# Kernel optimization log

Hardware: AMD Instinct MI355X
Metric: run time of the kernel (lower is better)

Reference implementation:

```python
import jax, jax.numpy as jnp
import numpy as np

# MANO fingertip / palm prior vertex indices from contact_loss
_F1 = [697,698,699,700,712,713,714,715,737,738,739,740,741,743,744,745,746,748,749,750,753,754,755,756,757,758,759,760,761,762,763,764,765,766,767,768]
_F2 = [46,47,48,49,164,165,166,167,194,195,223,237,238,280,281,298,301,317,320,323,324,325,326,327,328,329,330,331,332,333,340,341,342,343,344,345,346,347,348,349,350,351,352,353,354,355]
_F3 = [356,357,358,359,375,376,386,387,396,397,402,403,413,429,433,434,435,436,437,438,439,440,441,442,443,444,452,453,454,455,456,459,460,461,462,463,464,465,466,467]
_F4 = [468,469,470,471,484,485,486,496,497,506,507,513,514,524,545,546,547,548,549,550,551,552,553,555,563,564,565,566,567,570,572,573,574,575,576,577,578]
_F5 = [580,581,582,583,600,601,602,614,615,624,625,630,631,641,663,664,665,666,667,668,670,672,680,681,682,683,684,686,687,688,689,690,691,692,693,694,695]
_F0 = [73,96,98,99,772,774,775,777]
PRIOR_IDX = np.array(_F1 + _F2 + _F3 + _F4 + _F5 + _F0, dtype=np.int32)

KL_COEF = 0.005
A_W, B_W, C_W, D_W, E_W = 1.0, 0.1, 1000.0, 10.0, 10.0  # init kwargs a..e


def _nn(src, trg):
    """Brute-force 1-NN: src [B,N1,3] -> trg [B,N2,3].
    Returns (sq_dist [B,N1], idx [B,N1], diff src-near [B,N1,3])."""
    d2 = (jnp.sum(src * src, -1)[:, :, None]
          + jnp.sum(trg * trg, -1)[:, None, :]
          - 2.0 * jnp.einsum('bnd,bmd->bnm', src, trg))  # [B,N1,N2]
    idx = jnp.argmin(d2, axis=-1)
    near = jnp.take_along_axis(trg, idx[:, :, None], axis=1)
    diff = src - near
    return jnp.sum(diff * diff, axis=-1), idx, diff


def _p2p_signed(x, y, x_normals):
    """point2point_signed(x, y, x_normals): signed dist y->x, unsigned x->y."""
    _, yidx, y2x = _nn(y, x)  # nearest x for each y
    y_nn_normal = jnp.take_along_axis(x_normals, yidx[:, :, None], axis=1)
    in_out = jnp.sign(jnp.sum(y_nn_normal * y2x, axis=-1))
    y2x_signed = jnp.sqrt(jnp.sum(y2x * y2x, axis=-1)) * in_out  # [B,P2]
    _, _, x2y = _nn(x, y)  # nearest y for each x
    x2y_dist = jnp.sqrt(jnp.sum(x2y * x2y, axis=-1))  # [B,P1]
    return y2x_signed, x2y_dist


def _forward(recon_xyz, gt_xyz, recon_normals, gt_normals, obj_xyz, mean, log_var, v_weights):
    B = recon_xyz.shape[0]
    f32 = recon_xyz.dtype
    # --- CVAE recon (L2) + KLD ---
    recon_loss = jnp.sum((recon_xyz - gt_xyz) ** 2) / B
    kld = -0.5 * jnp.sum(1.0 + log_var - mean ** 2 - jnp.exp(log_var)) / B * 10.0
    # --- obj -> hand NN (squared dists, pytorch3d knn_points convention) ---
    recon_d2, recon_idx, _ = _nn(obj_xyz, recon_xyz)  # [B,3000]
    gt_d2, _, _ = _nn(obj_xyz, gt_xyz)
    # --- contact map from GT NN dist thresholding ---
    cmap = jnp.sqrt(gt_d2) < 0.005  # [B,3000] bool
    # --- contact_loss: obj NN to prior (fingertip/palm) recon verts ---
    prior = recon_xyz[:, PRIOR_IDX, :]
    obj_cd, _, _ = _nn(obj_xyz, prior)
    n_pts = jnp.sum(cmap.astype(f32))
    contact = 3000.0 * jnp.where(n_pts > 0, jnp.sum(obj_cd * cmap) / (B * n_pts), 0.0)
    # --- CMap_consistency_loss ---
    recon_cmap = jnp.sqrt(recon_d2) < 0.005
    consistency = -5.0 * jnp.sum((recon_cmap & cmap).astype(f32)) / (n_pts + 1e-4)
    # --- inter_penetr_loss: interior obj points via NN-normal dot sign ---
    nn_hand = jnp.take_along_axis(recon_xyz, recon_idx[:, :, None], axis=1)
    nn_normal = jnp.take_along_axis(recon_normals, recon_idx[:, :, None], axis=1)
    interior = jnp.sum((nn_hand - obj_xyz) * nn_normal, axis=-1) > 0
    penetr = 100.0 * jnp.sum(recon_d2 * interior) / B
    # --- loss_cnet: signed chamfer consistency ---
    vw2 = v_weights ** (1.0 / 2.5)
    o2h, h2o = _p2p_signed(recon_xyz, obj_xyz, recon_normals)
    o2h_gt, h2o_gt = _p2p_signed(gt_xyz, obj_xyz, gt_normals)
    w_dist = (o2h_gt < 0.01) & (o2h_gt > -0.005)
    w_neg = o2h < 0.0
    w = jnp.where(w_neg, 1.5, jnp.where(w_dist, 1.0, 0.1))
    loss_h = 35.0 * (1.0 - KL_COEF) * jnp.mean(jnp.abs(jnp.abs(h2o) - jnp.abs(h2o_gt)) * vw2)
    loss_o = 30.0 * (1.0 - KL_COEF) * jnp.mean(jnp.abs(o2h - o2h_gt) * w)
    cnet = loss_h + loss_o
    return (A_W * recon_loss + B_W * kld + C_W * penetr
            + D_W * contact + E_W * consistency + cnet)


def setup_inputs() -> dict:
    key = jax.random.key(0)
    ks = jax.random.split(key, 8)
    B, NH, NO, Z = 32, 778, 3000, 64
    s = 0.05  # meter-scale point clouds so contact thresholds (5mm) are meaningful
    def unit(k, shape):
        v = jax.random.normal(k, shape, dtype=jnp.float32)
        return v / jnp.linalg.norm(v, axis=-1, keepdims=True)
    return {
        'recon_xyz': jax.random.normal(ks[0], (B, NH, 3), dtype=jnp.float32) * s,
        'gt_xyz': jax.random.normal(ks[1], (B, NH, 3), dtype=jnp.float32) * s,
        'recon_normals': unit(ks[2], (B, NH, 3)),
        'gt_normals': unit(ks[3], (B, NH, 3)),
        'obj_xyz': jax.random.normal(ks[4], (B, NO, 3), dtype=jnp.float32) * s,
        'mean': jax.random.normal(ks[5], (B, Z), dtype=jnp.float32),
        'log_var': jax.random.normal(ks[6], (B, Z), dtype=jnp.float32) * 0.1,
        'v_weights': jax.random.uniform(ks[7], (NH,), dtype=jnp.float32),
    }


def reference(recon_xyz, gt_xyz, recon_normals, gt_normals, obj_xyz, mean, log_var, v_weights):
    return _forward(recon_xyz, gt_xyz, recon_normals, gt_normals, obj_xyz, mean, log_var, v_weights)
```

## Files before the change

### kernel.cpp

```cpp
#include <hip/hip_runtime.h>
#include <math.h>


#define NB 32
#define NH 778
#define NO 3000
#define NZ 64
#define NP 204

#define P_OBJ 4
#define OBJ_PTS 1024
#define OBJ_TILES 3

#define T2 12
#define FIN_OBJ_BLKS (NB * T2)
#define FIN_TAIL_BLKS ((NB * NH + 255) / 256)
#define FIN_BLKS (FIN_OBJ_BLKS + FIN_TAIL_BLKS)

#define NKEY (NB * NO)
#define NHT  (NB * NH)

#define ACC_STRIDE 32
#define ACC_SLOTS 16
#define ACC_FLOATS (ACC_SLOTS * ACC_STRIDE)

typedef unsigned int uint32;

__device__ __constant__ int c_prior[NP] = {
  697,698,699,700,712,713,714,715,737,738,739,740,741,743,744,745,746,748,749,750,
  753,754,755,756,757,758,759,760,761,762,763,764,765,766,767,768,
  46,47,48,49,164,165,166,167,194,195,223,237,238,280,281,298,301,317,320,323,
  324,325,326,327,328,329,330,331,332,333,340,341,342,343,344,345,346,347,348,349,
  350,351,352,353,354,355,
  356,357,358,359,375,376,386,387,396,397,402,403,413,429,433,434,435,436,437,438,
  439,440,441,442,443,444,452,453,454,455,456,459,460,461,462,463,464,465,466,467,
  468,469,470,471,484,485,486,496,497,506,507,513,514,524,545,546,547,548,549,550,
  551,552,553,555,563,564,565,566,567,570,572,573,574,575,576,577,578,
  580,581,582,583,600,601,602,614,615,624,625,630,631,641,663,664,665,666,667,668,
  670,672,680,681,682,683,684,686,687,688,689,690,691,692,693,694,695,
  73,96,98,99,772,774,775,777
};

__device__ __constant__ int c_prior_sorted[NP] = {
  46,47,48,49,73,96,98,99,164,165,166,167,194,
  195,223,237,238,280,281,298,301,317,320,323,324,325,326,327,328,329,330,331,
  332,333,340,341,342,343,344,345,346,347,348,349,350,351,352,353,354,355,356,
  357,358,359,375,376,386,387,
  396,397,402,403,413,429,433,434,435,436,437,438,439,440,441,442,443,444,452,
  453,454,455,456,459,460,461,462,463,464,465,466,467,468,469,470,471,484,485,
  486,496,497,506,507,513,514,524,545,546,547,548,549,550,551,552,553,555,563,
  564,565,566,567,570,572,573,574,575,576,577,578,580,581,582,583,
  600,601,602,614,615,624,625,630,631,641,663,664,665,666,667,668,670,672,680,
  681,682,683,684,686,687,688,689,690,691,692,693,694,695,697,698,699,700,712,
  713,714,715,737,738,739,740,741,743,744,745,746,748,749,750,753,754,755,756,
  757,758,759,760,761,762,763,764,765,766,767,768,772,774,775,777
};
__device__ __constant__ int c_psplit4[5] = {0, 13, 58, 131, 204};
__device__ __constant__ int c_psplit8[9] = {0, 6, 14, 19, 58, 97, 131, 154, 204};

__device__ inline float wave_sum(float v) {
  v += __shfl_down(v, 32);
  v += __shfl_down(v, 16);
  v += __shfl_down(v, 8);
  v += __shfl_down(v, 4);
  v += __shfl_down(v, 2);
  v += __shfl_down(v, 1);
  return v;
}

__device__ __forceinline__ float f_min3(float a, float b, float c) {
  float r;
  asm("v_min3_f32 %0, %1, %2, %3" : "=v"(r) : "v"(a), "v"(b), "v"(c));
  return r;
}
__device__ __forceinline__ float f_packao(float t, int j, uint32 mask) {
  float r;
  asm("v_and_or_b32 %0, %1, %2, %3" : "=v"(r) : "v"(t), "s"(mask), "v"(j));
  return r;
}

template<int JS, int JC, int HCn, int HCSn>
__global__ __launch_bounds__(256) void mega1t(
    const float* __restrict__ recon, const float* __restrict__ gt,
    const float* __restrict__ obj,
    float* __restrict__ keyR, float* __restrict__ keyG,
    float* __restrict__ priorK,
    float* __restrict__ minHR, float* __restrict__ minHG,
    float* __restrict__ accs)
{
  const int OBJ_B = NB * OBJ_TILES * JS;
  const int bid = blockIdx.x;
  const int tid = threadIdx.x;
  const uint32 KMASK = 0xFFFFFC00u;

  if (bid == 0) {
    accs[tid] = 0.0f;
    accs[tid + 256] = 0.0f;
  }

  if (bid < OBJ_B) {
    __shared__ float4 shA[JC];
    __shared__ float4 shB[JC];
    const int b     = bid / (OBJ_TILES * JS);
    const int rem   = bid % (OBJ_TILES * JS);
    const int tile  = rem / JS;
    const int split = rem % JS;
    const int jbase = split * JC;
    const int jcnt  = (NH - jbase < JC) ? (NH - jbase) : JC;

    for (int i = tid; i < jcnt; i += 256) {
      const float* p = recon + ((size_t)b * NH + jbase + i) * 3;
      float x = p[0], y = p[1], z = p[2];
      shA[i] = make_float4(x, y, z, x*x + y*y + z*z);
      const float* q = gt + ((size_t)b * NH + jbase + i) * 3;
      float gx = q[0], gy = q[1], gz = q[2];
      shB[i] = make_float4(gx, gy, gz, gx*gx + gy*gy + gz*gz);
    }
    __syncthreads();

    float nx[P_OBJ], ny[P_OBJ], nz[P_OBJ];
    int ob[P_OBJ]; bool val[P_OBJ];
    #pragma unroll
    for (int m = 0; m < P_OBJ; ++m) {
      int o = tile * OBJ_PTS + m * 256 + tid;
      ob[m] = o; val[m] = (o < NO);
      float x = 0.f, y = 0.f, z = 0.f;
      if (val[m]) {
        const float* op = obj + ((size_t)b * NO + o) * 3;
        x = op[0]; y = op[1]; z = op[2];
      }
      nx[m] = -2.f * x; ny[m] = -2.f * y; nz[m] = -2.f * z;
    }

    float bR[P_OBJ], bG[P_OBJ];
    #pragma unroll
    for (int m = 0; m < P_OBJ; ++m) { bR[m] = 3.4e38f; bG[m] = 3.4e38f; }

#define RSTEP(hh0, hh1, jj0, jj1) \
    { _Pragma("unroll") for (int m = 0; m < P_OBJ; ++m) { \
        float t0 = fmaf(nx[m], hh0.x, hh0.w); t0 = fmaf(ny[m], hh0.y, t0); t0 = fmaf(nz[m], hh0.z, t0); \
        float t1 = fmaf(nx[m], hh1.x, hh1.w); t1 = fmaf(ny[m], hh1.y, t1); t1 = fmaf(nz[m], hh1.z, t1); \
        bR[m] = f_min3(bR[m], f_packao(t0, jj0, KMASK), f_packao(t1, jj1, KMASK)); } }
#define GSTEP(gg0, gg1, jj0, jj1) \
    { _Pragma("unroll") for (int m = 0; m < P_OBJ; ++m) { \
        float u0 = fmaf(nx[m], gg0.x, gg0.w); u0 = fmaf(ny[m], gg0.y, u0); u0 = fmaf(nz[m], gg0.z, u0); \
        float u1 = fmaf(nx[m], gg1.x, gg1.w); u1 = fmaf(ny[m], gg1.y, u1); u1 = fmaf(nz[m], gg1.z, u1); \
        bG[m] = f_min3(bG[m], f_packao(u0, jj0, KMASK), f_packao(u1, jj1, KMASK)); } }

    float4 h0 = shA[0], h1 = shA[1];
    int i = 0;
    for (; i + 3 < jcnt; i += 2) {
      float4 g0 = shB[i], g1 = shB[i + 1];
      RSTEP(h0, h1, jbase + i, jbase + i + 1);
      float4 hn0 = shA[i + 2], hn1 = shA[i + 3];
      GSTEP(g0, g1, jbase + i, jbase + i + 1);
      h0 = hn0; h1 = hn1;
    }
    {
      float4 g0 = shB[i], g1 = shB[i + 1];
      RSTEP(h0, h1, jbase + i, jbase + i + 1);
      GSTEP(g0, g1, jbase + i, jbase + i + 1);
      i += 2;
    }
    for (; i < jcnt; ++i) {
      float4 hh = shA[i], gg = shB[i];
      #pragma unroll
      for (int m = 0; m < P_OBJ; ++m) {
        float t0 = fmaf(nx[m], hh.x, hh.w); t0 = fmaf(ny[m], hh.y, t0); t0 = fmaf(nz[m], hh.z, t0);
        bR[m] = fminf(bR[m], f_packao(t0, jbase + i, KMASK));
        float u0 = fmaf(nx[m], gg.x, gg.w); u0 = fmaf(ny[m], gg.y, u0); u0 = fmaf(nz[m], gg.z, u0);
        bG[m] = fminf(bG[m], f_packao(u0, jbase + i, KMASK));
      }
    }
#undef RSTEP
#undef GSTEP

    float bP[P_OBJ];
    #pragma unroll
    for (int m = 0; m < P_OBJ; ++m) bP[m] = 3.4e38f;
    const int* psp = (JS == 8) ? c_psplit8 : c_psplit4;
    const int pk0 = psp[split], pk1 = psp[split + 1];
    int k = pk0;
    for (; k + 1 < pk1; k += 2) {
      float4 ha = shA[c_prior_sorted[k] - jbase];
      float4 hb = shA[c_prior_sorted[k + 1] - jbase];
      #pragma unroll
      for (int m = 0; m < P_OBJ; ++m) {
        float t = fmaf(nx[m], ha.x, ha.w); t = fmaf(ny[m], ha.y, t); t = fmaf(nz[m], ha.z, t);
        float u = fmaf(nx[m], hb.x, hb.w); u = fmaf(ny[m], hb.y, u); u = fmaf(nz[m], hb.z, u);
        bP[m] = f_min3(bP[m], t, u);
      }
    }
    if (k < pk1) {
      float4 ha = shA[c_prior_sorted[k] - jbase];
      #pragma unroll
      for (int m = 0; m < P_OBJ; ++m) {
        float t = fmaf(nx[m], ha.x, ha.w); t = fmaf(ny[m], ha.y, t); t = fmaf(nz[m], ha.z, t);
        bP[m] = fminf(bP[m], t);
      }
    }

    #pragma unroll
    for (int m = 0; m < P_OBJ; ++m) {
      if (!val[m]) continue;
      const size_t idx = (size_t)split * NKEY + (size_t)b * NO + ob[m];
      keyR[idx] = bR[m];
      keyG[idx] = bG[m];
      priorK[idx] = bP[m];
    }
  } else {
    __shared__ float4 sO[HCSn];
    const int bid2 = bid - OBJ_B;
    const int oc = bid2 % HCn;
    const int b  = bid2 / HCn;

    const float* Ob = obj + ((size_t)b * NO + oc * HCSn) * 3;
    for (int i2 = tid; i2 < HCSn; i2 += 256) {
      float x = Ob[3*i2], y = Ob[3*i2+1], z = Ob[3*i2+2];
      sO[i2] = make_float4(x, y, z, x*x + y*y + z*z);
    }
    __syncthreads();

    float nrx[3], nry[3], nrz[3];
    float ngx[3], ngy[3], ngz[3];
    #pragma unroll
    for (int m = 0; m < 3; ++m) {
      const int j = m * 256 + tid;
      const float* rp = recon + ((size_t)b * NH + j) * 3;
      const float* gp = gt    + ((size_t)b * NH + j) * 3;
      nrx[m] = -2.f*rp[0]; nry[m] = -2.f*rp[1]; nrz[m] = -2.f*rp[2];
      ngx[m] = -2.f*gp[0]; ngy[m] = -2.f*gp[1]; ngz[m] = -2.f*gp[2];
    }

    float mR[3], mG[3];
    #pragma unroll
    for (int m = 0; m < 3; ++m) { mR[m] = 3.4e38f; mG[m] = 3.4e38f; }

#define HSTEP(oo0, oo1) \
    { _Pragma("unroll") for (int m = 0; m < 3; ++m) { \
        float t0 = fmaf(nrx[m], oo0.x, oo0.w); t0 = fmaf(nry[m], oo0.y, t0); t0 = fmaf(nrz[m], oo0.z, t0); \
        float t1 = fmaf(nrx[m], oo1.x, oo1.w); t1 = fmaf(nry[m], oo1.y, t1); t1 = fmaf(nrz[m], oo1.z, t1); \
        mR[m] = f_min3(mR[m], t0, t1); \
        float u0 = fmaf(ngx[m], oo0.x, oo0.w); u0 = fmaf(ngy[m], oo0.y, u0); u0 = fmaf(ngz[m], oo0.z, u0); \
        float u1 = fmaf(ngx[m], oo1.x, oo1.w); u1 = fmaf(ngy[m], oo1.y, u1); u1 = fmaf(ngz[m], oo1.z, u1); \
        mG[m] = f_min3(mG[m], u0, u1); } }

    float4 o0 = sO[0], o1 = sO[1];
    int k2 = 0;
    for (; k2 + 3 < HCSn; k2 += 2) {
      float4 a0 = sO[k2 + 2], a1 = sO[k2 + 3];
      HSTEP(o0, o1);
      o0 = a0; o1 = a1;
    }
    HSTEP(o0, o1);
    k2 += 2;
    for (; k2 < HCSn; ++k2) {
      float4 oc4 = sO[k2];
      #pragma unroll
      for (int m = 0; m < 3; ++m) {
        float t0 = fmaf(nrx[m], oc4.x, oc4.w); t0 = fmaf(nry[m], oc4.y, t0); t0 = fmaf(nrz[m], oc4.z, t0);
        mR[m] = fminf(mR[m], t0);
        float u0 = fmaf(ngx[m], oc4.x, oc4.w); u0 = fmaf(ngy[m], oc4.y, u0); u0 = fmaf(ngz[m], oc4.z, u0);
        mG[m] = fminf(mG[m], u0);
      }
    }
#undef HSTEP

    #pragma unroll
    for (int m = 0; m < 3; ++m) {
      const int j = m * 256 + tid;
      const size_t idx = (size_t)oc * NHT + (size_t)b * NH + j;
      minHR[idx] = mR[m];
      minHG[idx] = mG[m];
    }

    const int tw = bid2 & 3;
    if ((tid >> 6) == tw) {
      const int j3 = 768 + (tid & 63);
      const bool v3 = (j3 < NH);
      float rx=0.f,ry=0.f,rz=0.f,gx=0.f,gy=0.f,gz=0.f;
      if (v3) {
        const float* rp = recon + ((size_t)b * NH + j3) * 3;
        const float* gp = gt    + ((size_t)b * NH + j3) * 3;
        rx=rp[0];ry=rp[1];rz=rp[2]; gx=gp[0];gy=gp[1];gz=gp[2];
      }
      const float n3rx=-2.f*rx, n3ry=-2.f*ry, n3rz=-2.f*rz;
      const float n3gx=-2.f*gx, n3gy=-2.f*gy, n3gz=-2.f*gz;
      float m3R = 3.4e38f, m3G = 3.4e38f;
      int k3 = 0;
      for (; k3 + 1 < HCSn; k3 += 2) {
        float4 q0 = sO[k3], q1 = sO[k3 + 1];
        float t0 = fmaf(n3rx, q0.x, q0.w); t0 = fmaf(n3ry, q0.y, t0); t0 = fmaf(n3rz, q0.z, t0);
        float t1 = fmaf(n3rx, q1.x, q1.w); t1 = fmaf(n3ry, q1.y, t1); t1 = fmaf(n3rz, q1.z, t1);
        m3R = f_min3(m3R, t0, t1);
        float u0 = fmaf(n3gx, q0.x, q0.w); u0 = fmaf(n3gy, q0.y, u0); u0 = fmaf(n3gz, q0.z, u0);
        float u1 = fmaf(n3gx, q1.x, q1.w); u1 = fmaf(n3gy, q1.y, u1); u1 = fmaf(n3gz, q1.z, u1);
        m3G = f_min3(m3G, u0, u1);
      }
      if (HCSn & 1) {
        float4 q0 = sO[HCSn - 1];
        float t0 = fmaf(n3rx, q0.x, q0.w); t0 = fmaf(n3ry, q0.y, t0); t0 = fmaf(n3rz, q0.z, t0);
        m3R = fminf(m3R, t0);
        float u0 = fmaf(n3gx, q0.x, q0.w); u0 = fmaf(n3gy, q0.y, u0); u0 = fmaf(n3gz, q0.z, u0);
        m3G = fminf(m3G, u0);
      }
      if (v3) {
        const size_t idx = (size_t)oc * NHT + (size_t)b * NH + j3;
        minHR[idx] = m3R;
        minHG[idx] = m3G;
      }
    }
  }
}

template<int JS, int HCn>
__global__ __launch_bounds__(256) void mega2t(
    const float* __restrict__ recon, const float* __restrict__ gt,
    const float* __restrict__ rnorm, const float* __restrict__ gnorm,
    const float* __restrict__ obj,
    const float* __restrict__ mean, const float* __restrict__ logv,
    const float* __restrict__ vw,
    const float* __restrict__ keyR, const float* __restrict__ keyG,
    const float* __restrict__ priorK,
    const float* __restrict__ minHR, const float* __restrict__ minHG,
    float* __restrict__ accs, float* __restrict__ out)
{
  __shared__ float red[4][5];
  const int bid = blockIdx.x;
  const int tid = threadIdx.x;
  const int lane = tid & 63, wv = tid >> 6;

  if (bid < FIN_OBJ_BLKS) {
    const int b = bid / T2;
    const int tile = bid % T2;
    const int o = tile * 256 + tid;
    float penetr = 0.f, nptsv = 0.f, contactv = 0.f, consistv = 0.f, lossov = 0.f;
    if (o < NO) {
      const float* op = obj + ((size_t)b * NO + o) * 3;
      const float ox = op[0], oy = op[1], oz = op[2];
      const float o2 = ox*ox + oy*oy + oz*oz;
      const size_t base = (size_t)b * NO + o;

      float kR = 3.4e38f, kG = 3.4e38f, bP = 3.4e38f;
      #pragma unroll
      for (int s = 0; s < JS; ++s) {
        kR = fminf(kR, keyR[(size_t)s * NKEY + base]);
        kG = fminf(kG, keyG[(size_t)s * NKEY + base]);
        bP = fminf(bP, priorK[(size_t)s * NKEY + base]);
      }
      uint32 kRb = __float_as_uint(kR), kGb = __float_as_uint(kG);
      int idxR = (int)(kRb & 0x3FFu), idxG = (int)(kGb & 0x3FFu);
      float d2R = fmaxf(__uint_as_float(kRb & 0xFFFFFC00u) + o2, 0.f);
      float d2G = fmaxf(__uint_as_float(kGb & 0xFFFFFC00u) + o2, 0.f);
      float d2P = fmaxf(bP + o2, 0.f);

      const float* hR = recon + ((size_t)b * NH + idxR) * 3;
      const float* nR = rnorm + ((size_t)b * NH + idxR) * 3;
      float dotR = (ox - hR[0]) * nR[0] + (oy - hR[1]) * nR[1] + (oz - hR[2]) * nR[2];
      const float* hG = gt + ((size_t)b * NH + idxG) * 3;
      const float* nG = gnorm + ((size_t)b * NH + idxG) * 3;
      float dotG = (ox - hG[0]) * nG[0] + (oy - hG[1]) * nG[1] + (oz - hG[2]) * nG[2];

      float sgnR = (dotR > 0.f) ? 1.f : ((dotR < 0.f) ? -1.f : 0.f);
      float sgnG = (dotG > 0.f) ? 1.f : ((dotG < 0.f) ? -1.f : 0.f);
      float sR_ = sqrtf(d2R), sG_ = sqrtf(d2G);
      float o2h = sR_ * sgnR, o2hg = sG_ * sgnG;

      bool interior = dotR < 0.f;
      bool cmap = sG_ < 0.005f;
      bool rcmap = sR_ < 0.005f;

      penetr   = interior ? d2R : 0.f;
      nptsv    = cmap ? 1.f : 0.f;
      contactv = cmap ? d2P : 0.f;
      consistv = (cmap && rcmap) ? 1.f : 0.f;
      float w = (o2h < 0.f) ? 1.5f
              : (((o2hg < 0.01f) && (o2hg > -0.005f)) ? 1.f : 0.1f);
      lossov = fabsf(o2h - o2hg) * w;
    }

    float vals[5] = {penetr, nptsv, contactv, consistv, lossov};
    #pragma unroll
    for (int q = 0; q < 5; ++q) {
      float s = wave_sum(vals[q]);
      if (lane == 0) red[wv][q] = s;
    }
    __syncthreads();
    if (tid < 5) {
      float s = red[0][tid] + red[1][tid] + red[2][tid] + red[3][tid];
      atomicAdd(&accs[tid * ACC_STRIDE], s);
    }
  } else {
    const int t = (bid - FIN_OBJ_BLKS) * 256 + tid;
    float lossh = 0.f, rsum = 0.f, ksum = 0.f;
    if (t < NB * NH) {
      const float* rp = recon + (size_t)t * 3;
      const float* gp = gt + (size_t)t * 3;
      float rx = rp[0], ry = rp[1], rz = rp[2];
      float gx = gp[0], gy = gp[1], gz = gp[2];
      float d0 = rx - gx, d1 = ry - gy, d2 = rz - gz;
      rsum = d0*d0 + d1*d1 + d2*d2;

      float mRt = 3.4e38f, mGt = 3.4e38f;
      #pragma unroll
      for (int c = 0; c < HCn; ++c) {
        mRt = fminf(mRt, minHR[(size_t)c * NHT + t]);
        mGt = fminf(mGt, minHG[(size_t)c * NHT + t]);
      }
      float r2 = rx*rx + ry*ry + rz*rz;
      float g2 = gx*gx + gy*gy + gz*gz;
      float d2Rh = fmaxf(mRt + r2, 0.f);
      float d2Gh = fmaxf(mGt + g2, 0.f);
      int j = t % NH;
      lossh = fabsf(sqrtf(d2Rh) - sqrtf(d2Gh)) * powf(vw[j], 0.4f);
    }
    if (t < NB * NZ) {
      float m = mean[t], lv = logv[t];
      ksum = 1.f + lv - m * m - expf(lv);
    }
    float vals[3] = {lossh, rsum, ksum};
    #pragma unroll
    for (int q = 0; q < 3; ++q) {
      float s = wave_sum(vals[q]);
      if (lane == 0) red[wv][q] = s;
    }
    __syncthreads();
    if (tid < 3) {
      float s = red[0][tid] + red[1][tid] + red[2][tid] + red[3][tid];
      atomicAdd(&accs[(5 + tid) * ACC_STRIDE], s);
    }
  }

  __syncthreads();
  if (tid == 0) {
    __threadfence();
    int* cnt = (int*)(accs + 8 * ACC_STRIDE);
    int old = atomicAdd(cnt, 1);
    if (old == FIN_BLKS - 1) {
      float a[8];
      #pragma unroll
      for (int q = 0; q < 8; ++q) a[q] = atomicAdd(&accs[q * ACC_STRIDE], 0.0f);
      const float recon_loss = a[6] / (float)NB;
      const float kld = -0.5f * a[7] / (float)NB * 10.f;
      const float penetr = 100.f * a[0] / (float)NB;
      const float npts = a[1];
      const float contact = (npts > 0.f) ? (3000.f * a[2] / ((float)NB * npts)) : 0.f;
      const float consistency = -5.f * a[3] / (npts + 0.0001f);
      const float lossh = 35.f * (1.f - 0.005f) * (a[5] / (float)(NB * NH));
      const float losso = 30.f * (1.f - 0.005f) * (a[4] / (float)(NB * NO));
      out[0] = recon_loss + 0.1f * kld + 1000.f * penetr + 10.f * contact
             + 10.f * consistency + lossh + losso;
    }
  }
}

__global__ __launch_bounds__(256) void obj_mono(
    const float* __restrict__ recon, const float* __restrict__ gt,
    const float* __restrict__ rnorm, const float* __restrict__ gnorm,
    const float* __restrict__ obj, float* __restrict__ accs)
{
  __shared__ float4 sR[NH];
  __shared__ float4 sG[NH];
  __shared__ float red[4][5];
  const int b = blockIdx.x / 12;
  const int tile = blockIdx.x % 12;
  const int tid = threadIdx.x;
  for (int i = tid; i < NH; i += 256) {
    const float* p = recon + ((size_t)b * NH + i) * 3;
    float x = p[0], y = p[1], z = p[2];
    sR[i] = make_float4(x, y, z, x*x + y*y + z*z);
    const float* q = gt + ((size_t)b * NH + i) * 3;
    float gx = q[0], gy = q[1], gz = q[2];
    sG[i] = make_float4(gx, gy, gz, gx*gx + gy*gy + gz*gz);
  }
  __syncthreads();
  const int o = tile * 256 + tid;
  float penetr = 0.f, nptsv = 0.f, contactv = 0.f, consistv = 0.f, lossov = 0.f;
  if (o < NO) {
    const float* op = obj + ((size_t)b * NO + o) * 3;
    const float ox = op[0], oy = op[1], oz = op[2];
    const float nx = -2.f*ox, ny = -2.f*oy, nz = -2.f*oz;
    const float o2 = ox*ox + oy*oy + oz*oz;
    float bR = 3.4e38f, bG = 3.4e38f; int iR = 0, iG = 0;
    for (int i = 0; i < NH; ++i) {
      float4 h = sR[i];
      float t = fmaf(nx, h.x, h.w); t = fmaf(ny, h.y, t); t = fmaf(nz, h.z, t);
      if (t < bR) { bR = t; iR = i; }
      float4 g = sG[i];
      float u = fmaf(nx, g.x, g.w); u = fmaf(ny, g.y, u); u = fmaf(nz, g.z, u);
      if (u < bG) { bG = u; iG = i; }
    }
    float bP = 3.4e38f;
    for (int k = 0; k < NP; ++k) {
      float4 h = sR[c_prior[k]];
      float t = fmaf(nx, h.x, h.w); t = fmaf(ny, h.y, t); t = fmaf(nz, h.z, t);
      bP = fminf(bP, t);
    }
    float d2R = fmaxf(bR + o2, 0.f);
    float d2G = fmaxf(bG + o2, 0.f);
    float d2P = fmaxf(bP + o2, 0.f);
    float4 hR = sR[iR];
    const float* nR = rnorm + ((size_t)b * NH + iR) * 3;
    float dotR = (ox-hR.x)*nR[0] + (oy-hR.y)*nR[1] + (oz-hR.z)*nR[2];
    float4 hG = sG[iG];
    const float* nG = gnorm + ((size_t)b * NH + iG) * 3;
    float dotG = (ox-hG.x)*nG[0] + (oy-hG.y)*nG[1] + (oz-hG.z)*nG[2];
    float sgnR = (dotR > 0.f) ? 1.f : ((dotR < 0.f) ? -1.f : 0.f);
    float sgnG = (dotG > 0.f) ? 1.f : ((dotG < 0.f) ? -1.f : 0.f);
    float sR_ = sqrtf(d2R), sG_ = sqrtf(d2G);
    float o2h = sR_*sgnR, o2hg = sG_*sgnG;
    bool interior = dotR < 0.f;
    bool cmap = sG_ < 0.005f, rcmap = sR_ < 0.005f;
    penetr = interior ? d2R : 0.f;
    nptsv = cmap ? 1.f : 0.f;
    contactv = cmap ? d2P : 0.f;
    consistv = (cmap && rcmap) ? 1.f : 0.f;
    float w = (o2h < 0.f) ? 1.5f : (((o2hg < 0.01f) && (o2hg > -0.005f)) ? 1.f : 0.1f);
    lossov = fabsf(o2h - o2hg) * w;
  }
  float vals[5] = {penetr, nptsv, contactv, consistv, lossov};
  const int lane = tid & 63, wv = tid >> 6;
  for (int q = 0; q < 5; ++q) {
    float s = wave_sum(vals[q]);
    if (lane == 0) red[wv][q] = s;
  }
  __syncthreads();
  if (tid < 5) {
    float s = red[0][tid] + red[1][tid] + red[2][tid] + red[3][tid];
    atomicAdd(&accs[tid * ACC_STRIDE], s);
  }
}

__global__ __launch_bounds__(256) void hand_full(
    const float* __restrict__ recon, const float* __restrict__ gt,
    const float* __restrict__ obj, const float* __restrict__ vw,
    float* __restrict__ accs)
{
  __shared__ float4 sO[500];
  __shared__ float red[4];
  const int b = blockIdx.x >> 2;
  const int j = ((blockIdx.x & 3) << 8) + threadIdx.x;
  const bool valid = j < NH;
  float rx=0,ry=0,rz=0,gx=0,gy=0,gz=0;
  if (valid) {
    const float* rp = recon + ((size_t)b * NH + j) * 3;
    const float* gp = gt + ((size_t)b * NH + j) * 3;
    rx=rp[0];ry=rp[1];rz=rp[2]; gx=gp[0];gy=gp[1];gz=gp[2];
  }
  const float nrx=-2.f*rx, nry=-2.f*ry, nrz=-2.f*rz;
  const float ngx=-2.f*gx, ngy=-2.f*gy, ngz=-2.f*gz;
  const float r2 = rx*rx+ry*ry+rz*rz, g2 = gx*gx+gy*gy+gz*gz;
  float mR = 3.4e38f, mG = 3.4e38f;
  for (int oc = 0; oc < 6; ++oc) {
    __syncthreads();
    const float* Ob = obj + ((size_t)b * NO + oc * 500) * 3;
    for (int i = threadIdx.x; i < 500; i += 256) {
      float x = Ob[3*i], y = Ob[3*i+1], z = Ob[3*i+2];
      sO[i] = make_float4(x, y, z, x*x + y*y + z*z);
    }
    __syncthreads();
    if (valid) {
      for (int k = 0; k < 500; ++k) {
        float4 o4 = sO[k];
        float t = fmaf(nrx,o4.x,o4.w); t = fmaf(nry,o4.y,t); t = fmaf(nrz,o4.z,t);
        mR = fminf(mR, t);
        float u = fmaf(ngx,o4.x,o4.w); u = fmaf(ngy,o4.y,u); u = fmaf(ngz,o4.z,u);
        mG = fminf(mG, u);
      }
    }
  }
  float lossh = valid ? fabsf(sqrtf(fmaxf(mR+r2,0.f)) - sqrtf(fmaxf(mG+g2,0.f))) * powf(vw[j], 0.4f) : 0.f;
  const int lane = threadIdx.x & 63, wv = threadIdx.x >> 6;
  float s = wave_sum(lossh);
  if (lane == 0) red[wv] = s;
  __syncthreads();
  if (threadIdx.x == 0) atomicAdd(&accs[5 * ACC_STRIDE], red[0]+red[1]+red[2]+red[3]);
}

__global__ __launch_bounds__(256) void tail_nomins(
    const float* __restrict__ recon, const float* __restrict__ gt,
    const float* __restrict__ mean, const float* __restrict__ logv,
    float* __restrict__ accs)
{
  __shared__ float red[4][2];
  const int t = blockIdx.x * 256 + threadIdx.x;
  float rsum = 0.f, ksum = 0.f;
  if (t < NB * NH) {
    const float* rp = recon + (size_t)t * 3;
    const float* gp = gt + (size_t)t * 3;
    float d0 = rp[0]-gp[0], d1 = rp[1]-gp[1], d2 = rp[2]-gp[2];
    rsum = d0*d0 + d1*d1 + d2*d2;
  }
  if (t < NB * NZ) {
    float m = mean[t], lv = logv[t];
    ksum = 1.f + lv - m*m - expf(lv);
  }
  float vals[2] = {rsum, ksum};
  const int lane = threadIdx.x & 63, wv = threadIdx.x >> 6;
  for (int q = 0; q < 2; ++q) {
    float s = wave_sum(vals[q]);
    if (lane == 0) red[wv][q] = s;
  }
  __syncthreads();
  if (threadIdx.x < 2) {
    float s = red[0][threadIdx.x] + red[1][threadIdx.x] + red[2][threadIdx.x] + red[3][threadIdx.x];
    atomicAdd(&accs[(6 + threadIdx.x) * ACC_STRIDE], s);
  }
}

__global__ void init_small(float* accs) {
  int t = threadIdx.x;
  accs[t] = 0.0f;
  accs[t + 256] = 0.0f;
}

__global__ void final_fb(const float* __restrict__ a, float* __restrict__ out) {
  const float recon_loss = a[6 * ACC_STRIDE] / (float)NB;
  const float kld = -0.5f * a[7 * ACC_STRIDE] / (float)NB * 10.f;
  const float penetr = 100.f * a[0] / (float)NB;
  const float npts = a[1 * ACC_STRIDE];
  const float contact = (npts > 0.f) ? (3000.f * a[2 * ACC_STRIDE] / ((float)NB * npts)) : 0.f;
  const float consistency = -5.f * a[3 * ACC_STRIDE] / (npts + 0.0001f);
  const float lossh = 35.f * (1.f - 0.005f) * (a[5 * ACC_STRIDE] / (float)(NB * NH));
  const float losso = 30.f * (1.f - 0.005f) * (a[4 * ACC_STRIDE] / (float)(NB * NO));
  out[0] = recon_loss + 0.1f*kld + 1000.f*penetr + 10.f*contact + 10.f*consistency + lossh + losso;
}

extern "C" void kernel_launch(void* const* d_in, const int* in_sizes, int n_in,
                              void* d_out, int out_size, void* d_ws, size_t ws_size,
                              hipStream_t stream) {
  const float* recon = (const float*)d_in[0];
  const float* gt    = (const float*)d_in[1];
  const float* rnorm = (const float*)d_in[2];
  const float* gnorm = (const float*)d_in[3];
  const float* obj   = (const float*)d_in[4];
  const float* mean  = (const float*)d_in[5];
  const float* logv  = (const float*)d_in[6];
  const float* vw    = (const float*)d_in[7];
  float* out = (float*)d_out;

  float* accs = (float*)d_ws;
  float* base = (float*)((char*)d_ws + ACC_FLOATS * sizeof(float));

  const size_t neededB = ACC_FLOATS * sizeof(float)
                       + (3ull * 8 * NKEY + 2ull * 24 * NHT) * sizeof(float);
  const size_t neededA = ACC_FLOATS * sizeof(float)
                       + (3ull * 4 * NKEY + 2ull * 12 * NHT) * sizeof(float);

  if (ws_size >= neededB) {
    float* keyR   = base;
    float* keyG   = keyR + (size_t)8 * NKEY;
    float* priorK = keyG + (size_t)8 * NKEY;
    float* minHR  = priorK + (size_t)8 * NKEY;
    float* minHG  = minHR + (size_t)24 * NHT;
    const int g1 = NB * OBJ_TILES * 8 + NB * 24;
    mega1t<8, 98, 24, 125><<<g1, 256, 0, stream>>>(
        recon, gt, obj, keyR, keyG, priorK, minHR, minHG, accs);
    mega2t<8, 24><<<FIN_BLKS, 256, 0, stream>>>(
        recon, gt, rnorm, gnorm, obj, mean, logv, vw,
        keyR, keyG, priorK, minHR, minHG, accs, out);
  } else if (ws_size >= neededA) {
    float* keyR   = base;
    float* keyG   = keyR + (size_t)4 * NKEY;
    float* priorK = keyG + (size_t)4 * NKEY;
    float* minHR  = priorK + (size_t)4 * NKEY;
    float* minHG  = minHR + (size_t)12 * NHT;
    const int g1 = NB * OBJ_TILES * 4 + NB * 12;
    mega1t<4, 195, 12, 250><<<g1, 256, 0, stream>>>(
        recon, gt, obj, keyR, keyG, priorK, minHR, minHG, accs);
    mega2t<4, 12><<<FIN_BLKS, 256, 0, stream>>>(
        recon, gt, rnorm, gnorm, obj, mean, logv, vw,
        keyR, keyG, priorK, minHR, minHG, accs, out);
  } else {
    init_small<<<1, 256, 0, stream>>>(accs);
    obj_mono<<<NB * 12, 256, 0, stream>>>(recon, gt, rnorm, gnorm, obj, accs);
    hand_full<<<NB * 4, 256, 0, stream>>>(recon, gt, obj, vw, accs);
    tail_nomins<<<(NB * NH + 255) / 256, 256, 0, stream>>>(recon, gt, mean, logv, accs);
    final_fb<<<1, 1, 0, stream>>>(accs, out);
  }
}
```

Before: 118.8 us.

## Split fused NN kernel into separate object and hand kernels with larger per-thread tiles

Replaces the single heterogeneous mega1t kernel with two launches: obj_nn handles all 3000 object points per block (12 per thread) over a hand-vertex split, and hand_nn runs 128-thread blocks with 6 hand vertices per thread. This raises register-level reuse of shared-memory hand/object data and removes the branch divergence between block roles, but cuts the object-phase grid from 768 to 256 blocks and adds a kernel launch. The 4-way workspace fallback path is removed. Register pressure from 12-point accumulators may lower occupancy.

Result: slower. 142.1 us (+19.6%).

```diff
diff --git a/kernel.cpp b/kernel.cpp
--- a/kernel.cpp
+++ b/kernel.cpp
@@ -8,9 +8,12 @@
 #define NZ 64
 #define NP 204
 
-#define P_OBJ 4
-#define OBJ_PTS 1024
-#define OBJ_TILES 3
+#define JS8 8
+#define JC8 98
+#define PO 12
+#define HC24 24
+#define HCS24 125
+#define PH 6
 
 #define T2 12
 #define FIN_OBJ_BLKS (NB * T2)
@@ -21,8 +24,7 @@
 #define NHT  (NB * NH)
 
 #define ACC_STRIDE 32
-#define ACC_SLOTS 16
-#define ACC_FLOATS (ACC_SLOTS * ACC_STRIDE)
+#define ACC_FLOATS 512
 
 typedef unsigned int uint32;
 
@@ -55,7 +57,6 @@
   713,714,715,737,738,739,740,741,743,744,745,746,748,749,750,753,754,755,756,
   757,758,759,760,761,762,763,764,765,766,767,768,772,774,775,777
 };
-__device__ __constant__ int c_psplit4[5] = {0, 13, 58, 131, 204};
 __device__ __constant__ int c_psplit8[9] = {0, 6, 14, 19, 58, 97, 131, 154, 204};
 
 __device__ inline float wave_sum(float v) {
@@ -79,16 +80,14 @@
   return r;
 }
 
-template<int JS, int JC, int HCn, int HCSn>
-__global__ __launch_bounds__(256) void mega1t(
+__global__ __launch_bounds__(256) void obj_nn(
     const float* __restrict__ recon, const float* __restrict__ gt,
     const float* __restrict__ obj,
     float* __restrict__ keyR, float* __restrict__ keyG,
-    float* __restrict__ priorK,
-    float* __restrict__ minHR, float* __restrict__ minHG,
-    float* __restrict__ accs)
+    float* __restrict__ priorK, float* __restrict__ accs)
 {
-  const int OBJ_B = NB * OBJ_TILES * JS;
+  __shared__ float4 shA[JC8];
+  __shared__ float4 shB[JC8];
   const int bid = blockIdx.x;
   const int tid = threadIdx.x;
   const uint32 KMASK = 0xFFFFFC00u;
@@ -98,217 +97,196 @@
     accs[tid + 256] = 0.0f;
   }
 
-  if (bid < OBJ_B) {
-    __shared__ float4 shA[JC];
-    __shared__ float4 shB[JC];
-    const int b     = bid / (OBJ_TILES * JS);
-    const int rem   = bid % (OBJ_TILES * JS);
-    const int tile  = rem / JS;
-    const int split = rem % JS;
-    const int jbase = split * JC;
-    const int jcnt  = (NH - jbase < JC) ? (NH - jbase) : JC;
-
-    for (int i = tid; i < jcnt; i += 256) {
-      const float* p = recon + ((size_t)b * NH + jbase + i) * 3;
-      float x = p[0], y = p[1], z = p[2];
-      shA[i] = make_float4(x, y, z, x*x + y*y + z*z);
-      const float* q = gt + ((size_t)b * NH + jbase + i) * 3;
-      float gx = q[0], gy = q[1], gz = q[2];
-      shB[i] = make_float4(gx, gy, gz, gx*gx + gy*gy + gz*gz);
-    }
-    __syncthreads();
-
-    float nx[P_OBJ], ny[P_OBJ], nz[P_OBJ];
-    int ob[P_OBJ]; bool val[P_OBJ];
-    #pragma unroll
-    for (int m = 0; m < P_OBJ; ++m) {
-      int o = tile * OBJ_PTS + m * 256 + tid;
-      ob[m] = o; val[m] = (o < NO);
-      float x = 0.f, y = 0.f, z = 0.f;
-      if (val[m]) {
-        const float* op = obj + ((size_t)b * NO + o) * 3;
-        x = op[0]; y = op[1]; z = op[2];
-      }
-      nx[m] = -2.f * x; ny[m] = -2.f * y; nz[m] = -2.f * z;
-    }
-
-    float bR[P_OBJ], bG[P_OBJ];
-    #pragma unroll
-    for (int m = 0; m < P_OBJ; ++m) { bR[m] = 3.4e38f; bG[m] = 3.4e38f; }
-
-#define RSTEP(hh0, hh1, jj0, jj1) \
-    { _Pragma("unroll") for (int m = 0; m < P_OBJ; ++m) { \
-        float t0 = fmaf(nx[m], hh0.x, hh0.w); t0 = fmaf(ny[m], hh0.y, t0); t0 = fmaf(nz[m], hh0.z, t0); \
-        float t1 = fmaf(nx[m], hh1.x, hh1.w); t1 = fmaf(ny[m], hh1.y, t1); t1 = fmaf(nz[m], hh1.z, t1); \
-        bR[m] = f_min3(bR[m], f_packao(t0, jj0, KMASK), f_packao(t1, jj1, KMASK)); } }
-#define GSTEP(gg0, gg1, jj0, jj1) \
-    { _Pragma("unroll") for (int m = 0; m < P_OBJ; ++m) { \
-        float u0 = fmaf(nx[m], gg0.x, gg0.w); u0 = fmaf(ny[m], gg0.y, u0); u0 = fmaf(nz[m], gg0.z, u0); \
-        float u1 = fmaf(nx[m], gg1.x, gg1.w); u1 = fmaf(ny[m], gg1.y, u1); u1 = fmaf(nz[m], gg1.z, u1); \
-        bG[m] = f_min3(bG[m], f_packao(u0, jj0, KMASK), f_packao(u1, jj1, KMASK)); } }
-
-    float4 h0 = shA[0], h1 = shA[1];
-    int i = 0;
-    for (; i + 3 < jcnt; i += 2) {
-      float4 g0 = shB[i], g1 = shB[i + 1];
-      RSTEP(h0, h1, jbase + i, jbase + i + 1);
-      float4 hn0 = shA[i + 2], hn1 = shA[i + 3];
-      GSTEP(g0, g1, jbase + i, jbase + i + 1);
-      h0 = hn0; h1 = hn1;
+  const int b     = bid >> 3;
+  const int split = bid & 7;
+  const int jbase = split * JC8;
+  const int jcnt  = (NH - jbase < JC8) ? (NH - jbase) : JC8;
+
+  for (int i = tid; i < jcnt; i += 256) {
+    const float* p = recon + ((size_t)b * NH + jbase + i) * 3;
+    float x = p[0], y = p[1], z = p[2];
+    shA[i] = make_float4(x, y, z, x*x + y*y + z*z);
+    const float* q = gt + ((size_t)b * NH + jbase + i) * 3;
+    float gx = q[0], gy = q[1], gz = q[2];
+    shB[i] = make_float4(gx, gy, gz, gx*gx + gy*gy + gz*gz);
+  }
+  __syncthreads();
+
+  float nx[PO], ny[PO], nz[PO];
+  bool val[PO];
+  #pragma unroll
+  for (int m = 0; m < PO; ++m) {
+    const int o = m * 256 + tid;
+    val[m] = (o < NO);
+    float x = 0.f, y = 0.f, z = 0.f;
+    if (val[m]) {
+      const float* op = obj + ((size_t)b * NO + o) * 3;
+      x = op[0]; y = op[1]; z = op[2];
+    }
+    nx[m] = -2.f * x; ny[m] = -2.f * y; nz[m] = -2.f * z;
+  }
+
+  float bR[PO], bG[PO], bP[PO];
+  #pragma unroll
+  for (int m = 0; m < PO; ++m) { bR[m] = 3.4e38f; bG[m] = 3.4e38f; bP[m] = 3.4e38f; }
+
+  int i = 0;
+  for (; i + 1 < jcnt; i += 2) {
+    const int j0 = jbase + i, j1 = jbase + i + 1;
+    float4 h0 = shA[i], h1 = shA[i + 1];
+    float4 g0 = shB[i], g1 = shB[i + 1];
+    #pragma unroll
+    for (int m = 0; m < PO; ++m) {
+      float t0 = fmaf(nx[m], h0.x, h0.w); t0 = fmaf(ny[m], h0.y, t0); t0 = fmaf(nz[m], h0.z, t0);
+      float t1 = fmaf(nx[m], h1.x, h1.w); t1 = fmaf(ny[m], h1.y, t1); t1 = fmaf(nz[m], h1.z, t1);
+      bR[m] = f_min3(bR[m], f_packao(t0, j0, KMASK), f_packao(t1, j1, KMASK));
+      float u0 = fmaf(nx[m], g0.x, g0.w); u0 = fmaf(ny[m], g0.y, u0); u0 = fmaf(nz[m], g0.z, u0);
+      float u1 = fmaf(nx[m], g1.x, g1.w); u1 = fmaf(ny[m], g1.y, u1); u1 = fmaf(nz[m], g1.z, u1);
+      bG[m] = f_min3(bG[m], f_packao(u0, j0, KMASK), f_packao(u1, j1, KMASK));
+    }
+  }
+  if (i < jcnt) {
+    const int j0 = jbase + i;
+    float4 h0 = shA[i], g0 = shB[i];
+    #pragma unroll
+    for (int m = 0; m < PO; ++m) {
+      float t0 = fmaf(nx[m], h0.x, h0.w); t0 = fmaf(ny[m], h0.y, t0); t0 = fmaf(nz[m], h0.z, t0);
+      bR[m] = fminf(bR[m], f_packao(t0, j0, KMASK));
+      float u0 = fmaf(nx[m], g0.x, g0.w); u0 = fmaf(ny[m], g0.y, u0); u0 = fmaf(nz[m], g0.z, u0);
+      bG[m] = fminf(bG[m], f_packao(u0, j0, KMASK));
+    }
+  }
+
+  const int pk0 = c_psplit8[split], pk1 = c_psplit8[split + 1];
+  int k = pk0;
+  for (; k + 1 < pk1; k += 2) {
+    float4 ha = shA[c_prior_sorted[k] - jbase];
+    float4 hb = shA[c_prior_sorted[k + 1] - jbase];
+    #pragma unroll
+    for (int m = 0; m < PO; ++m) {
+      float t = fmaf(nx[m], ha.x, ha.w); t = fmaf(ny[m], ha.y, t); t = fmaf(nz[m], ha.z, t);
+      float u = fmaf(nx[m], hb.x, hb.w); u = fmaf(ny[m], hb.y, u); u = fmaf(nz[m], hb.z, u);
+      bP[m] = f_min3(bP[m], t, u);
+    }
+  }
+  if (k < pk1) {
+    float4 ha = shA[c_prior_sorted[k] - jbase];
+    #pragma unroll
+    for (int m = 0; m < PO; ++m) {
+      float t = fmaf(nx[m], ha.x, ha.w); t = fmaf(ny[m], ha.y, t); t = fmaf(nz[m], ha.z, t);
+      bP[m] = fminf(bP[m], t);
+    }
+  }
+
+  #pragma unroll
+  for (int m = 0; m < PO; ++m) {
+    if (!val[m]) continue;
+    const size_t idx = (size_t)split * NKEY + (size_t)b * NO + (m * 256 + tid);
+    keyR[idx] = bR[m];
+    keyG[idx] = bG[m];
+    priorK[idx] = bP[m];
+  }
+}
+
+__global__ __launch_bounds__(128) void hand_nn(
+    const float* __restrict__ recon, const float* __restrict__ gt,
+    const float* __restrict__ obj,
+    float* __restrict__ minHR, float* __restrict__ minHG)
+{
+  __shared__ float4 sO[HCS24];
+  const int bid = blockIdx.x;
+  const int tid = threadIdx.x;
+  const int oc = bid % HC24;
+  const int b  = bid / HC24;
+
+  const float* Ob = obj + ((size_t)b * NO + oc * HCS24) * 3;
+  for (int i = tid; i < HCS24; i += 128) {
+    float x = Ob[3*i], y = Ob[3*i+1], z = Ob[3*i+2];
+    sO[i] = make_float4(x, y, z, x*x + y*y + z*z);
+  }
+  __syncthreads();
+
+  float nrx[PH], nry[PH], nrz[PH];
+  float ngx[PH], ngy[PH], ngz[PH];
+  #pragma unroll
+  for (int m = 0; m < PH; ++m) {
+    const int j = m * 128 + tid;
+    const float* rp = recon + ((size_t)b * NH + j) * 3;
+    const float* gp = gt    + ((size_t)b * NH + j) * 3;
+    nrx[m] = -2.f*rp[0]; nry[m] = -2.f*rp[1]; nrz[m] = -2.f*rp[2];
+    ngx[m] = -2.f*gp[0]; ngy[m] = -2.f*gp[1]; ngz[m] = -2.f*gp[2];
+  }
+
+  float mR[PH], mG[PH];
+  #pragma unroll
+  for (int m = 0; m < PH; ++m) { mR[m] = 3.4e38f; mG[m] = 3.4e38f; }
+
+  int k = 0;
+  for (; k + 1 < HCS24; k += 2) {
+    float4 o0 = sO[k], o1 = sO[k + 1];
+    #pragma unroll
+    for (int m = 0; m < PH; ++m) {
+      float t0 = fmaf(nrx[m], o0.x, o0.w); t0 = fmaf(nry[m], o0.y, t0); t0 = fmaf(nrz[m], o0.z, t0);
+      float t1 = fmaf(nrx[m], o1.x, o1.w); t1 = fmaf(nry[m], o1.y, t1); t1 = fmaf(nrz[m], o1.z, t1);
+      mR[m] = f_min3(mR[m], t0, t1);
+      float u0 = fmaf(ngx[m], o0.x, o0.w); u0 = fmaf(ngy[m], o0.y, u0); u0 = fmaf(ngz[m], o0.z, u0);
+      float u1 = fmaf(ngx[m], o1.x, o1.w); u1 = fmaf(ngy[m], o1.y, u1); u1 = fmaf(ngz[m], o1.z, u1);
+      mG[m] = f_min3(mG[m], u0, u1);
+    }
+  }
+  {
+    float4 o0 = sO[HCS24 - 1];
+    #pragma unroll
+    for (int m = 0; m < PH; ++m) {
+      float t0 = fmaf(nrx[m], o0.x, o0.w); t0 = fmaf(nry[m], o0.y, t0); t0 = fmaf(nrz[m], o0.z, t0);
+      mR[m] = fminf(mR[m], t0);
+      float u0 = fmaf(ngx[m], o0.x, o0.w); u0 = fmaf(ngy[m], o0.y, u0); u0 = fmaf(ngz[m], o0.z, u0);
+      mG[m] = fminf(mG[m], u0);
+    }
+  }
+
+  #pragma unroll
+  for (int m = 0; m < PH; ++m) {
+    const int j = m * 128 + tid;
+    const size_t idx = (size_t)oc * NHT + (size_t)b * NH + j;
+    minHR[idx] = mR[m];
+    minHG[idx] = mG[m];
+  }
+
+  const int tw = bid & 1;
+  if ((tid >> 6) == tw) {
+    const int j3 = 768 + (tid & 63);
+    const bool v3 = (j3 < NH);
+    float rx=0.f,ry=0.f,rz=0.f,gx=0.f,gy=0.f,gz=0.f;
+    if (v3) {
+      const float* rp = recon + ((size_t)b * NH + j3) * 3;
+      const float* gp = gt    + ((size_t)b * NH + j3) * 3;
+      rx=rp[0];ry=rp[1];rz=rp[2]; gx=gp[0];gy=gp[1];gz=gp[2];
+    }
+    const float n3rx=-2.f*rx, n3ry=-2.f*ry, n3rz=-2.f*rz;
+    const float n3gx=-2.f*gx, n3gy=-2.f*gy, n3gz=-2.f*gz;
+    float m3R = 3.4e38f, m3G = 3.4e38f;
+    int k3 = 0;
+    for (; k3 + 1 < HCS24; k3 += 2) {
+      float4 q0 = sO[k3], q1 = sO[k3 + 1];
+      float t0 = fmaf(n3rx, q0.x, q0.w); t0 = fmaf(n3ry, q0.y, t0); t0 = fmaf(n3rz, q0.z, t0);
+      float t1 = fmaf(n3rx, q1.x, q1.w); t1 = fmaf(n3ry, q1.y, t1); t1 = fmaf(n3rz, q1.z, t1);
+      m3R = f_min3(m3R, t0, t1);
+      float u0 = fmaf(n3gx, q0.x, q0.w); u0 = fmaf(n3gy, q0.y, u0); u0 = fmaf(n3gz, q0.z, u0);
+      float u1 = fmaf(n3gx, q1.x, q1.w); u1 = fmaf(n3gy, q1.y, u1); u1 = fmaf(n3gz, q1.z, u1);
+      m3G = f_min3(m3G, u0, u1);
     }
     {
-      float4 g0 = shB[i], g1 = shB[i + 1];
-      RSTEP(h0, h1, jbase + i, jbase + i + 1);
-      GSTEP(g0, g1, jbase + i, jbase + i + 1);
-      i += 2;
-    }
-    for (; i < jcnt; ++i) {
-      float4 hh = shA[i], gg = shB[i];
-      #pragma unroll
-      for (int m = 0; m < P_OBJ; ++m) {
-        float t0 = fmaf(nx[m], hh.x, hh.w); t0 = fmaf(ny[m], hh.y, t0); t0 = fmaf(nz[m], hh.z, t0);
-        bR[m] = fminf(bR[m], f_packao(t0, jbase + i, KMASK));
-        float u0 = fmaf(nx[m], gg.x, gg.w); u0 = fmaf(ny[m], gg.y, u0); u0 = fmaf(nz[m], gg.z, u0);
-        bG[m] = fminf(bG[m], f_packao(u0, jbase + i, KMASK));
-      }
-    }
-#undef RSTEP
-#undef GSTEP
-
-    float bP[P_OBJ];
-    #pragma unroll
-    for (int m = 0; m < P_OBJ; ++m) bP[m] = 3.4e38f;
-    const int* psp = (JS == 8) ? c_psplit8 : c_psplit4;
-    const int pk0 = psp[split], pk1 = psp[split + 1];
-    int k = pk0;
-    for (; k + 1 < pk1; k += 2) {
-      float4 ha = shA[c_prior_sorted[k] - jbase];
-      float4 hb = shA[c_prior_sorted[k + 1] - jbase];
-      #pragma unroll
-      for (int m = 0; m < P_OBJ; ++m) {
-        float t = fmaf(nx[m], ha.x, ha.w); t = fmaf(ny[m], ha.y, t); t = fmaf(nz[m], ha.z, t);
-        float u = fmaf(nx[m], hb.x, hb.w); u = fmaf(ny[m], hb.y, u); u = fmaf(nz[m], hb.z, u);
-        bP[m] = f_min3(bP[m], t, u);
-      }
-    }
-    if (k < pk1) {
-      float4 ha = shA[c_prior_sorted[k] - jbase];
-      #pragma unroll
-      for (int m = 0; m < P_OBJ; ++m) {
-        float t = fmaf(nx[m], ha.x, ha.w); t = fmaf(ny[m], ha.y, t); t = fmaf(nz[m], ha.z, t);
-        bP[m] = fminf(bP[m], t);
-      }
-    }
-
-    #pragma unroll
-    for (int m = 0; m < P_OBJ; ++m) {
-      if (!val[m]) continue;
-      const size_t idx = (size_t)split * NKEY + (size_t)b * NO + ob[m];
-      keyR[idx] = bR[m];
-      keyG[idx] = bG[m];
-      priorK[idx] = bP[m];
-    }
-  } else {
-    __shared__ float4 sO[HCSn];
-    const int bid2 = bid - OBJ_B;
-    const int oc = bid2 % HCn;
-    const int b  = bid2 / HCn;
-
-    const float* Ob = obj + ((size_t)b * NO + oc * HCSn) * 3;
-    for (int i2 = tid; i2 < HCSn; i2 += 256) {
-      float x = Ob[3*i2], y = Ob[3*i2+1], z = Ob[3*i2+2];
-      sO[i2] = make_float4(x, y, z, x*x + y*y + z*z);
-    }
-    __syncthreads();
-
-    float nrx[3], nry[3], nrz[3];
-    float ngx[3], ngy[3], ngz[3];
-    #pragma unroll
-    for (int m = 0; m < 3; ++m) {
-      const int j = m * 256 + tid;
-      const float* rp = recon + ((size_t)b * NH + j) * 3;
-      const float* gp = gt    + ((size_t)b * NH + j) * 3;
-      nrx[m] = -2.f*rp[0]; nry[m] = -2.f*rp[1]; nrz[m] = -2.f*rp[2];
-      ngx[m] = -2.f*gp[0]; ngy[m] = -2.f*gp[1]; ngz[m] = -2.f*gp[2];
-    }
-
-    float mR[3], mG[3];
-    #pragma unroll
-    for (int m = 0; m < 3; ++m) { mR[m] = 3.4e38f; mG[m] = 3.4e38f; }
-
-#define HSTEP(oo0, oo1) \
-    { _Pragma("unroll") for (int m = 0; m < 3; ++m) { \
-        float t0 = fmaf(nrx[m], oo0.x, oo0.w); t0 = fmaf(nry[m], oo0.y, t0); t0 = fmaf(nrz[m], oo0.z, t0); \
-        float t1 = fmaf(nrx[m], oo1.x, oo1.w); t1 = fmaf(nry[m], oo1.y, t1); t1 = fmaf(nrz[m], oo1.z, t1); \
-        mR[m] = f_min3(mR[m], t0, t1); \
-        float u0 = fmaf(ngx[m], oo0.x, oo0.w); u0 = fmaf(ngy[m], oo0.y, u0); u0 = fmaf(ngz[m], oo0.z, u0); \
-        float u1 = fmaf(ngx[m], oo1.x, oo1.w); u1 = fmaf(ngy[m], oo1.y, u1); u1 = fmaf(ngz[m], oo1.z, u1); \
-        mG[m] = f_min3(mG[m], u0, u1); } }
-
-    float4 o0 = sO[0], o1 = sO[1];
-    int k2 = 0;
-    for (; k2 + 3 < HCSn; k2 += 2) {
-      float4 a0 = sO[k2 + 2], a1 = sO[k2 + 3];
-      HSTEP(o0, o1);
-      o0 = a0; o1 = a1;
-    }
-    HSTEP(o0, o1);
-    k2 += 2;
-    for (; k2 < HCSn; ++k2) {
-      float4 oc4 = sO[k2];
-      #pragma unroll
-      for (int m = 0; m < 3; ++m) {
-        float t0 = fmaf(nrx[m], oc4.x, oc4.w); t0 = fmaf(nry[m], oc4.y, t0); t0 = fmaf(nrz[m], oc4.z, t0);
-        mR[m] = fminf(mR[m], t0);
-        float u0 = fmaf(ngx[m], oc4.x, oc4.w); u0 = fmaf(ngy[m], oc4.y, u0); u0 = fmaf(ngz[m], oc4.z, u0);
-        mG[m] = fminf(mG[m], u0);
-      }
-    }
-#undef HSTEP
-
-    #pragma unroll
-    for (int m = 0; m < 3; ++m) {
-      const int j = m * 256 + tid;
-      const size_t idx = (size_t)oc * NHT + (size_t)b * NH + j;
-      minHR[idx] = mR[m];
-      minHG[idx] = mG[m];
-    }
-
-    const int tw = bid2 & 3;
-    if ((tid >> 6) == tw) {
-      const int j3 = 768 + (tid & 63);
-      const bool v3 = (j3 < NH);
-      float rx=0.f,ry=0.f,rz=0.f,gx=0.f,gy=0.f,gz=0.f;
-      if (v3) {
-        const float* rp = recon + ((size_t)b * NH + j3) * 3;
-        const float* gp = gt    + ((size_t)b * NH + j3) * 3;
-        rx=rp[0];ry=rp[1];rz=rp[2]; gx=gp[0];gy=gp[1];gz=gp[2];
-      }
-      const float n3rx=-2.f*rx, n3ry=-2.f*ry, n3rz=-2.f*rz;
-      const float n3gx=-2.f*gx, n3gy=-2.f*gy, n3gz=-2.f*gz;
-      float m3R = 3.4e38f, m3G = 3.4e38f;
-      int k3 = 0;
-      for (; k3 + 1 < HCSn; k3 += 2) {
-        float4 q0 = sO[k3], q1 = sO[k3 + 1];
-        float t0 = fmaf(n3rx, q0.x, q0.w); t0 = fmaf(n3ry, q0.y, t0); t0 = fmaf(n3rz, q0.z, t0);
-        float t1 = fmaf(n3rx, q1.x, q1.w); t1 = fmaf(n3ry, q1.y, t1); t1 = fmaf(n3rz, q1.z, t1);
-        m3R = f_min3(m3R, t0, t1);
-        float u0 = fmaf(n3gx, q0.x, q0.w); u0 = fmaf(n3gy, q0.y, u0); u0 = fmaf(n3gz, q0.z, u0);
-        float u1 = fmaf(n3gx, q1.x, q1.w); u1 = fmaf(n3gy, q1.y, u1); u1 = fmaf(n3gz, q1.z, u1);
-        m3G = f_min3(m3G, u0, u1);
-      }
-      if (HCSn & 1) {
-        float4 q0 = sO[HCSn - 1];
-        float t0 = fmaf(n3rx, q0.x, q0.w); t0 = fmaf(n3ry, q0.y, t0); t0 = fmaf(n3rz, q0.z, t0);
-        m3R = fminf(m3R, t0);
-        float u0 = fmaf(n3gx, q0.x, q0.w); u0 = fmaf(n3gy, q0.y, u0); u0 = fmaf(n3gz, q0.z, u0);
-        m3G = fminf(m3G, u0);
-      }
-      if (v3) {
-        const size_t idx = (size_t)oc * NHT + (size_t)b * NH + j3;
-        minHR[idx] = m3R;
-        minHG[idx] = m3G;
-      }
+      float4 q0 = sO[HCS24 - 1];
+      float t0 = fmaf(n3rx, q0.x, q0.w); t0 = fmaf(n3ry, q0.y, t0); t0 = fmaf(n3rz, q0.z, t0);
+      m3R = fminf(m3R, t0);
+      float u0 = fmaf(n3gx, q0.x, q0.w); u0 = fmaf(n3gy, q0.y, u0); u0 = fmaf(n3gz, q0.z, u0);
+      m3G = fminf(m3G, u0);
+    }
+    if (v3) {
+      const size_t idx = (size_t)oc * NHT + (size_t)b * NH + j3;
+      minHR[idx] = m3R;
+      minHG[idx] = m3G;
     }
   }
 }
@@ -642,33 +620,20 @@
   float* accs = (float*)d_ws;
   float* base = (float*)((char*)d_ws + ACC_FLOATS * sizeof(float));
 
-  const size_t neededB = ACC_FLOATS * sizeof(float)
-                       + (3ull * 8 * NKEY + 2ull * 24 * NHT) * sizeof(float);
-  const size_t neededA = ACC_FLOATS * sizeof(float)
-                       + (3ull * 4 * NKEY + 2ull * 12 * NHT) * sizeof(float);
-
-  if (ws_size >= neededB) {
+  const size_t needed = ACC_FLOATS * sizeof(float)
+                      + (3ull * JS8 * NKEY + 2ull * HC24 * NHT) * sizeof(float);
+
+  if (ws_size >= needed) {
     float* keyR   = base;
-    float* keyG   = keyR + (size_t)8 * NKEY;
-    float* priorK = keyG + (size_t)8 * NKEY;
-    float* minHR  = priorK + (size_t)8 * NKEY;
-    float* minHG  = minHR + (size_t)24 * NHT;
-    const int g1 = NB * OBJ_TILES * 8 + NB * 24;
-    mega1t<8, 98, 24, 125><<<g1, 256, 0, stream>>>(
-        recon, gt, obj, keyR, keyG, priorK, minHR, minHG, accs);
-    mega2t<8, 24><<<FIN_BLKS, 256, 0, stream>>>(
-        recon, gt, rnorm, gnorm, obj, mean, logv, vw,
-        keyR, keyG, priorK, minHR, minHG, accs, out);
-  } else if (ws_size >= neededA) {
-    float* keyR   = base;
-    float* keyG   = keyR + (size_t)4 * NKEY;
-    float* priorK = keyG + (size_t)4 * NKEY;
-    float* minHR  = priorK + (size_t)4 * NKEY;
-    float* minHG  = minHR + (size_t)12 * NHT;
-    const int g1 = NB * OBJ_TILES * 4 + NB * 12;
-    mega1t<4, 195, 12, 250><<<g1, 256, 0, stream>>>(
-        recon, gt, obj, keyR, keyG, priorK, minHR, minHG, accs);
-    mega2t<4, 12><<<FIN_BLKS, 256, 0, stream>>>(
+    float* keyG   = keyR + (size_t)JS8 * NKEY;
+    float* priorK = keyG + (size_t)JS8 * NKEY;
+    float* minHR  = priorK + (size_t)JS8 * NKEY;
+    float* minHG  = minHR + (size_t)HC24 * NHT;
+    obj_nn<<<NB * JS8, 256, 0, stream>>>(
+        recon, gt, obj, keyR, keyG, priorK, accs);
+    hand_nn<<<NB * HC24, 128, 0, stream>>>(
+        recon, gt, obj, minHR, minHG);
+    mega2t<JS8, HC24><<<FIN_BLKS, 256, 0, stream>>>(
         recon, gt, rnorm, gnorm, obj, mean, logv, vw,
         keyR, keyG, priorK, minHR, minHG, accs, out);
   } else {
```
